# Optimization experiments

Measured on AMD Instinct MI355X. Metric: run time of the kernel, lower is better.

## Reference

```python
import jax, jax.numpy as jnp
import numpy as np

K = 3  # kernel size per dim


def _conv3d(x, w, b):
    # x: (N,C,T,H,W), w: (O,C,3,3,3), stride 1, padding 1
    y = jax.lax.conv_general_dilated(
        x, w, window_strides=(1, 1, 1),
        padding=((1, 1), (1, 1), (1, 1)),
        dimension_numbers=('NCDHW', 'OIDHW', 'NCDHW'))
    return y + b[None, :, None, None, None]


def _dcn_hw(x, w_off, b_off, w, b):
    """DeformConvPack_d with dimension='HW': offsets only along H and W."""
    N, C, T, H, W = x.shape
    KK = K * K * K  # 27 taps
    # offset prediction conv: (N, 2*27, T, H, W) -> (N, 27, 2, T, H, W)
    off = _conv3d(x, w_off, b_off).reshape(N, KK, 2, T, H, W)
    kt, kh, kw = [a.reshape(-1) for a in jnp.meshgrid(
        jnp.arange(K), jnp.arange(K), jnp.arange(K), indexing='ij')]
    # temporal sampling positions are integer (no offset along T)
    p_t = jnp.arange(T)[None, :] + kt[:, None] - 1              # (27, T)
    t_ok = ((p_t >= 0) & (p_t < T))[None, :, :, None, None]     # (1,27,T,1,1)
    p_tc = jnp.clip(p_t, 0, T - 1)[None, :, :, None, None]
    # fractional spatial sampling positions: (N,27,T,H,W)
    p_h = (jnp.arange(H, dtype=x.dtype)[None, None, None, :, None]
           + (kh - 1).astype(x.dtype)[None, :, None, None, None] + off[:, :, 0])
    p_w = (jnp.arange(W, dtype=x.dtype)[None, None, None, None, :]
           + (kw - 1).astype(x.dtype)[None, :, None, None, None] + off[:, :, 1])
    h0f = jnp.floor(p_h); w0f = jnp.floor(p_w)
    lh = (p_h - h0f)[..., None]; lw = (p_w - w0f)[..., None]
    h0 = h0f.astype(jnp.int32); w0 = w0f.astype(jnp.int32)
    xt = jnp.transpose(x, (0, 2, 3, 4, 1))  # (N,T,H,W,C) for gather
    bidx = jnp.arange(N)[:, None, None, None, None]

    def corner(hi, wi):
        ok = t_ok & (hi >= 0) & (hi < H) & (wi >= 0) & (wi < W)
        v = xt[bidx, p_tc, jnp.clip(hi, 0, H - 1), jnp.clip(wi, 0, W - 1)]
        return jnp.where(ok[..., None], v, jnp.zeros((), x.dtype))

    # bilinear interpolation with zero padding outside bounds
    samp = ((1 - lh) * (1 - lw)) * corner(h0, w0) \
         + ((1 - lh) * lw) * corner(h0, w0 + 1) \
         + (lh * (1 - lw)) * corner(h0 + 1, w0) \
         + (lh * lw) * corner(h0 + 1, w0 + 1)     # (N,27,T,H,W,C)
    O = w.shape[0]
    out = jnp.einsum('nkthwc,ock->nothw', samp, w.reshape(O, C, KK))
    return out + b[None, :, None, None, None]


def setup_inputs() -> dict:
    key = jax.random.key(0)
    ks = jax.random.split(key, 6)
    N, C, T, H, W = 1, 64, 7, 48, 48
    fan = 1.0 / np.sqrt(C * 27)
    return {
        'x': jax.random.normal(ks[0], (N, C, T, H, W), jnp.float32),
        'w_off0': jax.random.normal(ks[1], (54, C, 3, 3, 3), jnp.float32) * 0.01,
        'b_off0': jnp.zeros((54,), jnp.float32),
        'w0': jax.random.normal(ks[2], (C, C, 3, 3, 3), jnp.float32) * fan,
        'b0': jnp.zeros((C,), jnp.float32),
        'w_off1': jax.random.normal(ks[3], (54, C, 3, 3, 3), jnp.float32) * 0.01,
        'b_off1': jnp.zeros((54,), jnp.float32),
        'w1': jax.random.normal(ks[4], (C, C, 3, 3, 3), jnp.float32) * fan,
        'b1': jnp.zeros((C,), jnp.float32),
    }


def reference(x, w_off0, b_off0, w0, b0, w_off1, b_off1, w1, b1):
    h = _dcn_hw(x, w_off0, b_off0, w0, b0)
    h = jnp.where(h >= 0, h, 0.1 * h)  # LeakyReLU(0.1)
    return _dcn_hw(h, w_off1, b_off1, w1, b1) + x
```

## Files before the change

kernel.cpp:

```cpp
#include <hip/hip_runtime.h>

#define T_ 7
#define H_ 48
#define W_ 48
#define P_ 16128
#define HW_ 2304

typedef __attribute__((ext_vector_type(8))) short short8;
typedef __attribute__((ext_vector_type(4))) float f32x4;
typedef __attribute__((ext_vector_type(4))) unsigned u32x4;

__device__ __forceinline__ unsigned short f2bf(float f) {
  union { float f; unsigned u; } x{f};
  unsigned r = x.u + 0x7FFFu + ((x.u >> 16) & 1u);
  return (unsigned short)(r >> 16);
}
__device__ __forceinline__ float blo(unsigned u) {
  union { unsigned u; float f; } x{u << 16};
  return x.f;
}
__device__ __forceinline__ float bhi(unsigned u) {
  union { unsigned u; float f; } x{u & 0xFFFF0000u};
  return x.f;
}
__device__ __forceinline__ unsigned pack2(float a, float b) {
  return (unsigned)f2bf(a) | ((unsigned)f2bf(b) << 16);
}
__device__ __forceinline__ int xcd_swz(int bid, int nwg) {
  int cpx = nwg >> 3;
  return (bid & 7) * cpx + (bid >> 3);
}

__global__ void k_prep_x(const float* __restrict__ in, unsigned short* __restrict__ outb) {
  __shared__ float tile[64][65];
  int p0 = blockIdx.x * 64;
  int l = threadIdx.x & 63;
  int g = threadIdx.x >> 6;
#pragma unroll
  for (int i = 0; i < 16; ++i) {
    int c = g * 16 + i;
    tile[c][l] = in[c * P_ + p0 + l];
  }
  __syncthreads();
#pragma unroll
  for (int i = 0; i < 16; ++i) {
    int p = g * 16 + i;
    outb[(p0 + p) * 64 + l] = f2bf(tile[l][p]);
  }
}

__global__ void k_prep_w4(const float* __restrict__ s0, const float* __restrict__ s1,
                          const float* __restrict__ s2, const float* __restrict__ s3,
                          unsigned short* __restrict__ d0, unsigned short* __restrict__ d1,
                          unsigned short* __restrict__ d2, unsigned short* __restrict__ d3) {
  int y = blockIdx.y;
  const float* w = (y == 0) ? s0 : (y == 1) ? s1 : (y == 2) ? s2 : s3;
  unsigned short* wt = (y == 0) ? d0 : (y == 1) ? d1 : (y == 2) ? d2 : d3;
  int OC = (y < 2) ? 54 : 64;
  int idx = blockIdx.x * 256 + threadIdx.x;
  int j = idx & 7;
  int l = (idx >> 3) & 63;
  int kc = (idx >> 9) & 1;
  int nt = (idx >> 10) & 3;
  int k = idx >> 12;
  int o = nt * 16 + (l & 15);
  int c = kc * 32 + (l >> 4) * 8 + j;
  wt[idx] = (o < OC) ? f2bf(w[(o * 64 + c) * 27 + k]) : (unsigned short)0;
}

__global__ __launch_bounds__(256) void k_off4w(const unsigned short* __restrict__ xclb,
                                               const unsigned short* __restrict__ wAs,
                                               const float* __restrict__ boff,
                                               float* __restrict__ offt2) {
  __shared__ f32x4 red[4][4][64];
  int p0 = xcd_swz(blockIdx.x, gridDim.x) * 32;
  int t = p0 / HW_;
  int r0 = p0 - t * HW_;
  int h0r = r0 / W_;
  int w0s = r0 - h0r * W_;
  int h1r = h0r + (w0s == 32 ? 1 : 0);
  int w1s = (w0s == 32) ? 0 : w0s + 16;
  int tid = threadIdx.x;
  int lane = tid & 63, wid = tid >> 6;
  int pt = lane & 15, grp = lane >> 4;

  f32x4 zacc{0.f, 0.f, 0.f, 0.f};
  f32x4 aA0 = zacc, aA1 = zacc, aA2 = zacc, aA3 = zacc;
  f32x4 aB0 = zacc, aB1 = zacc, aB2 = zacc, aB3 = zacc;
  const short8 zero8{0, 0, 0, 0, 0, 0, 0, 0};
  int kbeg = wid * 7;

#pragma unroll
  for (int kk = 0; kk < 7; ++kk) {
    int kraw = kbeg + kk;
    int k = min(kraw, 26);
    int kt = k / 9;
    int r9 = k - kt * 9;
    int kh = r9 / 3;
    int kw = r9 - (r9 / 3) * 3;
    int t2 = t + kt - 1;
    bool tok = (kraw < 27) & ((unsigned)t2 < (unsigned)T_);
    int t2c = min(max(t2, 0), T_ - 1);

    const unsigned short* wp = wAs + (size_t)k * 4096 + lane * 8;
    short8 b00 = *(const short8*)(wp);
    short8 b01 = *(const short8*)(wp + 512);
    short8 b10 = *(const short8*)(wp + 1024);
    short8 b11 = *(const short8*)(wp + 1536);
    short8 b20 = *(const short8*)(wp + 2048);
    short8 b21 = *(const short8*)(wp + 2560);
    short8 b30 = *(const short8*)(wp + 3072);
    short8 b31 = *(const short8*)(wp + 3584);

    {
      int h2 = h0r + kh - 1;
      int w2 = w0s + pt + kw - 1;
      bool ok = tok & ((unsigned)h2 < (unsigned)H_) & ((unsigned)w2 < (unsigned)W_);
      int h2c = min(max(h2, 0), H_ - 1);
      int w2c = min(max(w2, 0), W_ - 1);
      const unsigned short* ap = xclb + ((size_t)(t2c * HW_ + h2c * W_ + w2c) * 64 + grp * 8);
      short8 a0 = *(const short8*)ap;
      short8 a1 = *(const short8*)(ap + 32);
      a0 = ok ? a0 : zero8;
      a1 = ok ? a1 : zero8;
      aA0 = __builtin_amdgcn_mfma_f32_16x16x32_bf16(a0, b00, aA0, 0, 0, 0);
      aA0 = __builtin_amdgcn_mfma_f32_16x16x32_bf16(a1, b01, aA0, 0, 0, 0);
      aA1 = __builtin_amdgcn_mfma_f32_16x16x32_bf16(a0, b10, aA1, 0, 0, 0);
      aA1 = __builtin_amdgcn_mfma_f32_16x16x32_bf16(a1, b11, aA1, 0, 0, 0);
      aA2 = __builtin_amdgcn_mfma_f32_16x16x32_bf16(a0, b20, aA2, 0, 0, 0);
      aA2 = __builtin_amdgcn_mfma_f32_16x16x32_bf16(a1, b21, aA2, 0, 0, 0);
      aA3 = __builtin_amdgcn_mfma_f32_16x16x32_bf16(a0, b30, aA3, 0, 0, 0);
      aA3 = __builtin_amdgcn_mfma_f32_16x16x32_bf16(a1, b31, aA3, 0, 0, 0);
    }
    {
      int h2 = h1r + kh - 1;
      int w2 = w1s + pt + kw - 1;
      bool ok = tok & ((unsigned)h2 < (unsigned)H_) & ((unsigned)w2 < (unsigned)W_);
      int h2c = min(max(h2, 0), H_ - 1);
      int w2c = min(max(w2, 0), W_ - 1);
      const unsigned short* ap = xclb + ((size_t)(t2c * HW_ + h2c * W_ + w2c) * 64 + grp * 8);
      short8 a0 = *(const short8*)ap;
      short8 a1 = *(const short8*)(ap + 32);
      a0 = ok ? a0 : zero8;
      a1 = ok ? a1 : zero8;
      aB0 = __builtin_amdgcn_mfma_f32_16x16x32_bf16(a0, b00, aB0, 0, 0, 0);
      aB0 = __builtin_amdgcn_mfma_f32_16x16x32_bf16(a1, b01, aB0, 0, 0, 0);
      aB1 = __builtin_amdgcn_mfma_f32_16x16x32_bf16(a0, b10, aB1, 0, 0, 0);
      aB1 = __builtin_amdgcn_mfma_f32_16x16x32_bf16(a1, b11, aB1, 0, 0, 0);
      aB2 = __builtin_amdgcn_mfma_f32_16x16x32_bf16(a0, b20, aB2, 0, 0, 0);
      aB2 = __builtin_amdgcn_mfma_f32_16x16x32_bf16(a1, b21, aB2, 0, 0, 0);
      aB3 = __builtin_amdgcn_mfma_f32_16x16x32_bf16(a0, b30, aB3, 0, 0, 0);
      aB3 = __builtin_amdgcn_mfma_f32_16x16x32_bf16(a1, b31, aB3, 0, 0, 0);
    }
  }

  int oc = wid * 16 + pt;
  float bb = (oc < 54) ? boff[oc] : 0.f;
  int kidx = oc >> 1, d = oc & 1;

  red[wid][0][lane] = aA0;
  red[wid][1][lane] = aA1;
  red[wid][2][lane] = aA2;
  red[wid][3][lane] = aA3;
  __syncthreads();
  {
    f32x4 s = red[0][wid][lane];
    s = s + red[1][wid][lane];
    s = s + red[2][wid][lane];
    s = s + red[3][wid][lane];
    if (oc < 54) {
#pragma unroll
      for (int r = 0; r < 4; ++r) {
        int p = p0 + grp * 4 + r;
        offt2[((size_t)kidx * P_ + p) * 2 + d] = s[r] + bb;
      }
    }
  }
  __syncthreads();
  red[wid][0][lane] = aB0;
  red[wid][1][lane] = aB1;
  red[wid][2][lane] = aB2;
  red[wid][3][lane] = aB3;
  __syncthreads();
  {
    f32x4 s = red[0][wid][lane];
    s = s + red[1][wid][lane];
    s = s + red[2][wid][lane];
    s = s + red[3][wid][lane];
    if (oc < 54) {
#pragma unroll
      for (int r = 0; r < 4; ++r) {
        int p = p0 + 16 + grp * 4 + r;
        offt2[((size_t)kidx * P_ + p) * 2 + d] = s[r] + bb;
      }
    }
  }
}

template <int MODE>
__global__ __launch_bounds__(256) void k_samp4w(
    const unsigned short* __restrict__ xclb, const float* __restrict__ offt2,
    const unsigned short* __restrict__ wBs, const float* __restrict__ bias,
    const float* __restrict__ resid, float* __restrict__ out32,
    unsigned short* __restrict__ outb) {
  __shared__ f32x4 red[4][4][64];
  __shared__ unsigned short sA[4][2][16][72];
  int p0 = xcd_swz(blockIdx.x, gridDim.x) * 32;
  int t = p0 / HW_;
  int r0 = p0 - t * HW_;
  int h0r = r0 / W_;
  int w0s = r0 - h0r * W_;
  int h1r = h0r + (w0s == 32 ? 1 : 0);
  int w1s = (w0s == 32) ? 0 : w0s + 16;
  int tid = threadIdx.x;
  int lane = tid & 63, wid = tid >> 6;
  int pt = lane & 15, grp = lane >> 4;

  f32x4 zacc{0.f, 0.f, 0.f, 0.f};
  f32x4 aA0 = zacc, aA1 = zacc, aA2 = zacc, aA3 = zacc;
  f32x4 aB0 = zacc, aB1 = zacc, aB2 = zacc, aB3 = zacc;
  int kbeg = wid * 7;

#pragma unroll
  for (int kk = 0; kk < 7; ++kk) {
    int kraw = kbeg + kk;
    int k = min(kraw, 26);
    int kt = k / 9;
    int r9 = k - kt * 9;
    int kh = r9 / 3;
    int kw = r9 - (r9 / 3) * 3;
    int t2 = t + kt - 1;
    bool tok = (kraw < 27) & ((unsigned)t2 < (unsigned)T_);
    int t2c = min(max(t2, 0), T_ - 1);

    const unsigned short* wp = wBs + (size_t)k * 4096 + lane * 8;
    short8 b00 = *(const short8*)(wp);
    short8 b01 = *(const short8*)(wp + 512);
    short8 b10 = *(const short8*)(wp + 1024);
    short8 b11 = *(const short8*)(wp + 1536);
    short8 b20 = *(const short8*)(wp + 2048);
    short8 b21 = *(const short8*)(wp + 2560);
    short8 b30 = *(const short8*)(wp + 3072);
    short8 b31 = *(const short8*)(wp + 3584);

#pragma unroll
    for (int f = 0; f < 2; ++f) {
      int hrow = (f == 0) ? h0r : h1r;
      int wst = (f == 0) ? w0s : w1s;
      float2 o2 = *(const float2*)(offt2 + ((size_t)k * P_ + p0 + f * 16 + pt) * 2);
      float ph = (float)(hrow + kh - 1) + o2.x;
      float pw = (float)(wst + pt + kw - 1) + o2.y;
      float hf = floorf(ph), wf = floorf(pw);
      float lh = ph - hf, lw = pw - wf;
      int h0 = (int)hf, w0i = (int)wf;
      int h1 = h0 + 1, w1 = w0i + 1;
      bool h0ok = ((unsigned)h0 < (unsigned)H_), h1ok = ((unsigned)h1 < (unsigned)H_);
      bool w0ok = ((unsigned)w0i < (unsigned)W_), w1ok = ((unsigned)w1 < (unsigned)W_);
      int h0c = min(max(h0, 0), H_ - 1), h1c = min(max(h1, 0), H_ - 1);
      int w0c = min(max(w0i, 0), W_ - 1), w1c = min(max(w1, 0), W_ - 1);
      float omlh = 1.f - lh, omlw = 1.f - lw;
      float g00 = (tok & h0ok & w0ok) ? omlh * omlw : 0.f;
      float g01 = (tok & h0ok & w1ok) ? omlh * lw : 0.f;
      float g10 = (tok & h1ok & w0ok) ? lh * omlw : 0.f;
      float g11 = (tok & h1ok & w1ok) ? lh * lw : 0.f;

      const unsigned short* bt = xclb + (size_t)(t2c * HW_) * 64 + grp * 16;
      int i00 = (h0c * W_ + w0c) * 64;
      int i01 = (h0c * W_ + w1c) * 64;
      int i10 = (h1c * W_ + w0c) * 64;
      int i11 = (h1c * W_ + w1c) * 64;
      u32x4 A0 = *(const u32x4*)(bt + i00), A1 = *(const u32x4*)(bt + i00 + 8);
      u32x4 B0 = *(const u32x4*)(bt + i01), B1 = *(const u32x4*)(bt + i01 + 8);
      u32x4 C0 = *(const u32x4*)(bt + i10), C1 = *(const u32x4*)(bt + i10 + 8);
      u32x4 D0 = *(const u32x4*)(bt + i11), D1 = *(const u32x4*)(bt + i11 + 8);

#define LERPU(a, b, c, d)                                                   \
  pack2(g00 * blo(a) + g01 * blo(b) + g10 * blo(c) + g11 * blo(d),          \
        g00 * bhi(a) + g01 * bhi(b) + g10 * bhi(c) + g11 * bhi(d))
      u32x4 v0, v1;
      v0[0] = LERPU(A0[0], B0[0], C0[0], D0[0]);
      v0[1] = LERPU(A0[1], B0[1], C0[1], D0[1]);
      v0[2] = LERPU(A0[2], B0[2], C0[2], D0[2]);
      v0[3] = LERPU(A0[3], B0[3], C0[3], D0[3]);
      v1[0] = LERPU(A1[0], B1[0], C1[0], D1[0]);
      v1[1] = LERPU(A1[1], B1[1], C1[1], D1[1]);
      v1[2] = LERPU(A1[2], B1[2], C1[2], D1[2]);
      v1[3] = LERPU(A1[3], B1[3], C1[3], D1[3]);
#undef LERPU

      __builtin_amdgcn_wave_barrier();
      *(u32x4*)&sA[wid][f][pt][grp * 16] = v0;
      *(u32x4*)&sA[wid][f][pt][grp * 16 + 8] = v1;
      __builtin_amdgcn_wave_barrier();

      short8 af0 = *(const short8*)&sA[wid][f][pt][grp * 8];
      short8 af1 = *(const short8*)&sA[wid][f][pt][32 + grp * 8];
      __builtin_amdgcn_wave_barrier();

      if (f == 0) {
        aA0 = __builtin_amdgcn_mfma_f32_16x16x32_bf16(af0, b00, aA0, 0, 0, 0);
        aA0 = __builtin_amdgcn_mfma_f32_16x16x32_bf16(af1, b01, aA0, 0, 0, 0);
        aA1 = __builtin_amdgcn_mfma_f32_16x16x32_bf16(af0, b10, aA1, 0, 0, 0);
        aA1 = __builtin_amdgcn_mfma_f32_16x16x32_bf16(af1, b11, aA1, 0, 0, 0);
        aA2 = __builtin_amdgcn_mfma_f32_16x16x32_bf16(af0, b20, aA2, 0, 0, 0);
        aA2 = __builtin_amdgcn_mfma_f32_16x16x32_bf16(af1, b21, aA2, 0, 0, 0);
        aA3 = __builtin_amdgcn_mfma_f32_16x16x32_bf16(af0, b30, aA3, 0, 0, 0);
        aA3 = __builtin_amdgcn_mfma_f32_16x16x32_bf16(af1, b31, aA3, 0, 0, 0);
      } else {
        aB0 = __builtin_amdgcn_mfma_f32_16x16x32_bf16(af0, b00, aB0, 0, 0, 0);
        aB0 = __builtin_amdgcn_mfma_f32_16x16x32_bf16(af1, b01, aB0, 0, 0, 0);
        aB1 = __builtin_amdgcn_mfma_f32_16x16x32_bf16(af0, b10, aB1, 0, 0, 0);
        aB1 = __builtin_amdgcn_mfma_f32_16x16x32_bf16(af1, b11, aB1, 0, 0, 0);
        aB2 = __builtin_amdgcn_mfma_f32_16x16x32_bf16(af0, b20, aB2, 0, 0, 0);
        aB2 = __builtin_amdgcn_mfma_f32_16x16x32_bf16(af1, b21, aB2, 0, 0, 0);
        aB3 = __builtin_amdgcn_mfma_f32_16x16x32_bf16(af0, b30, aB3, 0, 0, 0);
        aB3 = __builtin_amdgcn_mfma_f32_16x16x32_bf16(af1, b31, aB3, 0, 0, 0);
      }
    }
  }

  int ch = wid * 16 + pt;
  float bb = bias[ch];

  red[wid][0][lane] = aA0;
  red[wid][1][lane] = aA1;
  red[wid][2][lane] = aA2;
  red[wid][3][lane] = aA3;
  __syncthreads();
  {
    f32x4 s = red[0][wid][lane];
    s = s + red[1][wid][lane];
    s = s + red[2][wid][lane];
    s = s + red[3][wid][lane];
#pragma unroll
    for (int r = 0; r < 4; ++r) {
      int p = p0 + grp * 4 + r;
      float v = s[r] + bb;
      if (MODE == 0) {
        v = (v >= 0.f) ? v : 0.1f * v;
        outb[(size_t)p * 64 + ch] = f2bf(v);
      } else {
        out32[(size_t)ch * P_ + p] = v + resid[(size_t)ch * P_ + p];
      }
    }
  }
  __syncthreads();
  red[wid][0][lane] = aB0;
  red[wid][1][lane] = aB1;
  red[wid][2][lane] = aB2;
  red[wid][3][lane] = aB3;
  __syncthreads();
  {
    f32x4 s = red[0][wid][lane];
    s = s + red[1][wid][lane];
    s = s + red[2][wid][lane];
    s = s + red[3][wid][lane];
#pragma unroll
    for (int r = 0; r < 4; ++r) {
      int p = p0 + 16 + grp * 4 + r;
      float v = s[r] + bb;
      if (MODE == 0) {
        v = (v >= 0.f) ? v : 0.1f * v;
        outb[(size_t)p * 64 + ch] = f2bf(v);
      } else {
        out32[(size_t)ch * P_ + p] = v + resid[(size_t)ch * P_ + p];
      }
    }
  }
}

extern "C" void kernel_launch(void* const* d_in, const int* in_sizes, int n_in,
                              void* d_out, int out_size, void* d_ws, size_t ws_size,
                              hipStream_t stream) {
  const float* x      = (const float*)d_in[0];
  const float* w_off0 = (const float*)d_in[1];
  const float* b_off0 = (const float*)d_in[2];
  const float* w0     = (const float*)d_in[3];
  const float* b0     = (const float*)d_in[4];
  const float* w_off1 = (const float*)d_in[5];
  const float* b_off1 = (const float*)d_in[6];
  const float* w1     = (const float*)d_in[7];
  const float* b1     = (const float*)d_in[8];
  float* out = (float*)d_out;

  char* base = (char*)d_ws;
  unsigned short* x_clb = (unsigned short*)base;
  unsigned short* h_clb = (unsigned short*)(base + 2064384);
  float*          offt2 = (float*)(base + 4128768);
  unsigned short* wA0   = (unsigned short*)(base + 7612416);
  unsigned short* wA1   = (unsigned short*)(base + 7833600);
  unsigned short* wB0   = (unsigned short*)(base + 8054784);
  unsigned short* wB1   = (unsigned short*)(base + 8275968);

  hipLaunchKernelGGL(k_prep_x, dim3(252), dim3(256), 0, stream, x, x_clb);
  hipLaunchKernelGGL(k_prep_w4, dim3(432, 4), dim3(256), 0, stream,
                     w_off0, w_off1, w0, w1, wA0, wA1, wB0, wB1);

  hipLaunchKernelGGL(k_off4w, dim3(504), dim3(256), 0, stream, x_clb, wA0, b_off0, offt2);
  hipLaunchKernelGGL((k_samp4w<0>), dim3(504), dim3(256), 0, stream,
                     x_clb, offt2, wB0, b0, (const float*)nullptr, (float*)nullptr, h_clb);

  hipLaunchKernelGGL(k_off4w, dim3(504), dim3(256), 0, stream, h_clb, wA1, b_off1, offt2);
  hipLaunchKernelGGL((k_samp4w<1>), dim3(504), dim3(256), 0, stream,
                     h_clb, offt2, wB1, b1, x, out, (unsigned short*)nullptr);
}
```

Measured before the change: 99.67 us.

## Stage input row window in LDS for deformable sampling gathers

The sampling kernel now loops over the temporal tap, and for each one it cooperatively loads an 11-row by 48-column window of the bf16 input (all 64 channels) into dynamic shared memory with an XOR swizzle. The bilinear corner gathers then read from LDS, falling back to global loads only when a sampled row lies outside the window. Taps are redistributed so waves 0-2 each handle two spatial taps and wave 3 handles three. Per-tap offsets are preloaded, and the MFMA and weight loads are factored into helpers. The aim is to replace scattered global and L2 gathers with LDS reads, at the cost of about 66 KB of LDS per block, extra block barriers, lower occupancy and uneven work across waves.

```diff
diff --git a/kernel.cpp b/kernel.cpp
--- a/kernel.cpp
+++ b/kernel.cpp
@@ -5,6 +5,8 @@
 #define W_ 48
 #define P_ 16128
 #define HW_ 2304
+#define WR_ 11
+#define NCH_ (WR_ * 48 * 8)
 
 typedef __attribute__((ext_vector_type(8))) short short8;
 typedef __attribute__((ext_vector_type(4))) float f32x4;
@@ -29,6 +31,34 @@
 __device__ __forceinline__ int xcd_swz(int bid, int nwg) {
   int cpx = nwg >> 3;
   return (bid & 7) * cpx + (bid >> 3);
+}
+
+struct Wgt { short8 b00, b01, b10, b11, b20, b21, b30, b31; };
+
+__device__ __forceinline__ Wgt load_w(const unsigned short* base, int k, int lane) {
+  const unsigned short* wp = base + (size_t)k * 4096 + lane * 8;
+  Wgt w;
+  w.b00 = *(const short8*)(wp);
+  w.b01 = *(const short8*)(wp + 512);
+  w.b10 = *(const short8*)(wp + 1024);
+  w.b11 = *(const short8*)(wp + 1536);
+  w.b20 = *(const short8*)(wp + 2048);
+  w.b21 = *(const short8*)(wp + 2560);
+  w.b30 = *(const short8*)(wp + 3072);
+  w.b31 = *(const short8*)(wp + 3584);
+  return w;
+}
+
+__device__ __forceinline__ void mfma8(const Wgt& W, short8 af0, short8 af1,
+                                      f32x4& c0, f32x4& c1, f32x4& c2, f32x4& c3) {
+  c0 = __builtin_amdgcn_mfma_f32_16x16x32_bf16(af0, W.b00, c0, 0, 0, 0);
+  c0 = __builtin_amdgcn_mfma_f32_16x16x32_bf16(af1, W.b01, c0, 0, 0, 0);
+  c1 = __builtin_amdgcn_mfma_f32_16x16x32_bf16(af0, W.b10, c1, 0, 0, 0);
+  c1 = __builtin_amdgcn_mfma_f32_16x16x32_bf16(af1, W.b11, c1, 0, 0, 0);
+  c2 = __builtin_amdgcn_mfma_f32_16x16x32_bf16(af0, W.b20, c2, 0, 0, 0);
+  c2 = __builtin_amdgcn_mfma_f32_16x16x32_bf16(af1, W.b21, c2, 0, 0, 0);
+  c3 = __builtin_amdgcn_mfma_f32_16x16x32_bf16(af0, W.b30, c3, 0, 0, 0);
+  c3 = __builtin_amdgcn_mfma_f32_16x16x32_bf16(af1, W.b31, c3, 0, 0, 0);
 }
 
 __global__ void k_prep_x(const float* __restrict__ in, unsigned short* __restrict__ outb) {
@@ -102,16 +132,7 @@
     bool tok = (kraw < 27) & ((unsigned)t2 < (unsigned)T_);
     int t2c = min(max(t2, 0), T_ - 1);
 
-    const unsigned short* wp = wAs + (size_t)k * 4096 + lane * 8;
-    short8 b00 = *(const short8*)(wp);
-    short8 b01 = *(const short8*)(wp + 512);
-    short8 b10 = *(const short8*)(wp + 1024);
-    short8 b11 = *(const short8*)(wp + 1536);
-    short8 b20 = *(const short8*)(wp + 2048);
-    short8 b21 = *(const short8*)(wp + 2560);
-    short8 b30 = *(const short8*)(wp + 3072);
-    short8 b31 = *(const short8*)(wp + 3584);
-
+    Wgt W = load_w(wAs, k, lane);
     {
       int h2 = h0r + kh - 1;
       int w2 = w0s + pt + kw - 1;
@@ -123,14 +144,7 @@
       short8 a1 = *(const short8*)(ap + 32);
       a0 = ok ? a0 : zero8;
       a1 = ok ? a1 : zero8;
-      aA0 = __builtin_amdgcn_mfma_f32_16x16x32_bf16(a0, b00, aA0, 0, 0, 0);
-      aA0 = __builtin_amdgcn_mfma_f32_16x16x32_bf16(a1, b01, aA0, 0, 0, 0);
-      aA1 = __builtin_amdgcn_mfma_f32_16x16x32_bf16(a0, b10, aA1, 0, 0, 0);
-      aA1 = __builtin_amdgcn_mfma_f32_16x16x32_bf16(a1, b11, aA1, 0, 0, 0);
-      aA2 = __builtin_amdgcn_mfma_f32_16x16x32_bf16(a0, b20, aA2, 0, 0, 0);
-      aA2 = __builtin_amdgcn_mfma_f32_16x16x32_bf16(a1, b21, aA2, 0, 0, 0);
-      aA3 = __builtin_amdgcn_mfma_f32_16x16x32_bf16(a0, b30, aA3, 0, 0, 0);
-      aA3 = __builtin_amdgcn_mfma_f32_16x16x32_bf16(a1, b31, aA3, 0, 0, 0);
+      mfma8(W, a0, a1, aA0, aA1, aA2, aA3);
     }
     {
       int h2 = h1r + kh - 1;
@@ -143,14 +157,7 @@
       short8 a1 = *(const short8*)(ap + 32);
       a0 = ok ? a0 : zero8;
       a1 = ok ? a1 : zero8;
-      aB0 = __builtin_amdgcn_mfma_f32_16x16x32_bf16(a0, b00, aB0, 0, 0, 0);
-      aB0 = __builtin_amdgcn_mfma_f32_16x16x32_bf16(a1, b01, aB0, 0, 0, 0);
-      aB1 = __builtin_amdgcn_mfma_f32_16x16x32_bf16(a0, b10, aB1, 0, 0, 0);
-      aB1 = __builtin_amdgcn_mfma_f32_16x16x32_bf16(a1, b11, aB1, 0, 0, 0);
-      aB2 = __builtin_amdgcn_mfma_f32_16x16x32_bf16(a0, b20, aB2, 0, 0, 0);
-      aB2 = __builtin_amdgcn_mfma_f32_16x16x32_bf16(a1, b21, aB2, 0, 0, 0);
-      aB3 = __builtin_amdgcn_mfma_f32_16x16x32_bf16(a0, b30, aB3, 0, 0, 0);
-      aB3 = __builtin_amdgcn_mfma_f32_16x16x32_bf16(a1, b31, aB3, 0, 0, 0);
+      mfma8(W, a0, a1, aB0, aB1, aB2, aB3);
     }
   }
 
@@ -198,11 +205,12 @@
 }
 
 template <int MODE>
-__global__ __launch_bounds__(256) void k_samp4w(
+__global__ __launch_bounds__(256) void k_samp_st(
     const unsigned short* __restrict__ xclb, const float* __restrict__ offt2,
     const unsigned short* __restrict__ wBs, const float* __restrict__ bias,
     const float* __restrict__ resid, float* __restrict__ out32,
     unsigned short* __restrict__ outb) {
+  extern __shared__ u32x4 xs[];
   __shared__ f32x4 red[4][4][64];
   __shared__ unsigned short sA[4][2][16][72];
   int p0 = xcd_swz(blockIdx.x, gridDim.x) * 32;
@@ -212,6 +220,7 @@
   int w0s = r0 - h0r * W_;
   int h1r = h0r + (w0s == 32 ? 1 : 0);
   int w1s = (w0s == 32) ? 0 : w0s + 16;
+  int lo = h0r - 4;
   int tid = threadIdx.x;
   int lane = tid & 63, wid = tid >> 6;
   int pt = lane & 15, grp = lane >> 4;
@@ -219,102 +228,113 @@
   f32x4 zacc{0.f, 0.f, 0.f, 0.f};
   f32x4 aA0 = zacc, aA1 = zacc, aA2 = zacc, aA3 = zacc;
   f32x4 aB0 = zacc, aB1 = zacc, aB2 = zacc, aB3 = zacc;
-  int kbeg = wid * 7;
-
-#pragma unroll
-  for (int kk = 0; kk < 7; ++kk) {
-    int kraw = kbeg + kk;
-    int k = min(kraw, 26);
-    int kt = k / 9;
-    int r9 = k - kt * 9;
-    int kh = r9 / 3;
-    int kw = r9 - (r9 / 3) * 3;
+
+  for (int kt = 0; kt < 3; ++kt) {
     int t2 = t + kt - 1;
-    bool tok = (kraw < 27) & ((unsigned)t2 < (unsigned)T_);
+    bool tokt = (unsigned)t2 < (unsigned)T_;
     int t2c = min(max(t2, 0), T_ - 1);
 
-    const unsigned short* wp = wBs + (size_t)k * 4096 + lane * 8;
-    short8 b00 = *(const short8*)(wp);
-    short8 b01 = *(const short8*)(wp + 512);
-    short8 b10 = *(const short8*)(wp + 1024);
-    short8 b11 = *(const short8*)(wp + 1536);
-    short8 b20 = *(const short8*)(wp + 2048);
-    short8 b21 = *(const short8*)(wp + 2560);
-    short8 b30 = *(const short8*)(wp + 3072);
-    short8 b31 = *(const short8*)(wp + 3584);
-
-#pragma unroll
-    for (int f = 0; f < 2; ++f) {
-      int hrow = (f == 0) ? h0r : h1r;
-      int wst = (f == 0) ? w0s : w1s;
-      float2 o2 = *(const float2*)(offt2 + ((size_t)k * P_ + p0 + f * 16 + pt) * 2);
-      float ph = (float)(hrow + kh - 1) + o2.x;
-      float pw = (float)(wst + pt + kw - 1) + o2.y;
-      float hf = floorf(ph), wf = floorf(pw);
-      float lh = ph - hf, lw = pw - wf;
-      int h0 = (int)hf, w0i = (int)wf;
-      int h1 = h0 + 1, w1 = w0i + 1;
-      bool h0ok = ((unsigned)h0 < (unsigned)H_), h1ok = ((unsigned)h1 < (unsigned)H_);
-      bool w0ok = ((unsigned)w0i < (unsigned)W_), w1ok = ((unsigned)w1 < (unsigned)W_);
-      int h0c = min(max(h0, 0), H_ - 1), h1c = min(max(h1, 0), H_ - 1);
-      int w0c = min(max(w0i, 0), W_ - 1), w1c = min(max(w1, 0), W_ - 1);
-      float omlh = 1.f - lh, omlw = 1.f - lw;
-      float g00 = (tok & h0ok & w0ok) ? omlh * omlw : 0.f;
-      float g01 = (tok & h0ok & w1ok) ? omlh * lw : 0.f;
-      float g10 = (tok & h1ok & w0ok) ? lh * omlw : 0.f;
-      float g11 = (tok & h1ok & w1ok) ? lh * lw : 0.f;
-
-      const unsigned short* bt = xclb + (size_t)(t2c * HW_) * 64 + grp * 16;
-      int i00 = (h0c * W_ + w0c) * 64;
-      int i01 = (h0c * W_ + w1c) * 64;
-      int i10 = (h1c * W_ + w0c) * 64;
-      int i11 = (h1c * W_ + w1c) * 64;
-      u32x4 A0 = *(const u32x4*)(bt + i00), A1 = *(const u32x4*)(bt + i00 + 8);
-      u32x4 B0 = *(const u32x4*)(bt + i01), B1 = *(const u32x4*)(bt + i01 + 8);
-      u32x4 C0 = *(const u32x4*)(bt + i10), C1 = *(const u32x4*)(bt + i10 + 8);
-      u32x4 D0 = *(const u32x4*)(bt + i11), D1 = *(const u32x4*)(bt + i11 + 8);
+    float2 offp[3][2];
+#pragma unroll
+    for (int jj = 0; jj < 3; ++jj) {
+      int jcp = (wid < 3) ? (wid * 2 + min(jj, 1)) : (6 + jj);
+      size_t ob = ((size_t)(kt * 9 + jcp) * P_ + p0) * 2;
+      offp[jj][0] = *(const float2*)(offt2 + ob + (size_t)pt * 2);
+      offp[jj][1] = *(const float2*)(offt2 + ob + (size_t)(16 + pt) * 2);
+    }
+
+    __syncthreads();
+    for (int q = tid; q < NCH_; q += 256) {
+      int pidx = q >> 3;
+      int sub = q & 7;
+      int r = pidx / 48;
+      int c = pidx - r * 48;
+      int srow = min(max(lo + r, 0), H_ - 1);
+      const u32x4* src = (const u32x4*)(xclb + (size_t)(t2c * HW_ + srow * W_ + c) * 64);
+      xs[q ^ (pidx & 7)] = src[sub];
+    }
+    __syncthreads();
+
+#pragma unroll
+    for (int jj = 0; jj < 3; ++jj) {
+      bool ok_tap = (wid == 3) | (jj < 2);
+      if (ok_tap) {
+        int jc = (wid < 3) ? (wid * 2 + jj) : (6 + jj);
+        int kh = jc / 3;
+        int kw = jc - kh * 3;
+        int kk = kt * 9 + jc;
+        Wgt W = load_w(wBs, kk, lane);
+#pragma unroll
+        for (int f = 0; f < 2; ++f) {
+          int hrow = f ? h1r : h0r;
+          int wst = f ? w1s : w0s;
+          float2 o2 = offp[jj][f];
+          float ph = (float)(hrow + kh - 1) + o2.x;
+          float pw = (float)(wst + pt + kw - 1) + o2.y;
+          float hf = floorf(ph), wf = floorf(pw);
+          float lh = ph - hf, lw = pw - wf;
+          int h0 = (int)hf, w0i = (int)wf;
+          int h1 = h0 + 1, w1 = w0i + 1;
+          bool h0ok = ((unsigned)h0 < (unsigned)H_), h1ok = ((unsigned)h1 < (unsigned)H_);
+          bool w0ok = ((unsigned)w0i < (unsigned)W_), w1ok = ((unsigned)w1 < (unsigned)W_);
+          int h0c = min(max(h0, 0), H_ - 1), h1c = min(max(h1, 0), H_ - 1);
+          int w0c = min(max(w0i, 0), W_ - 1), w1c = min(max(w1, 0), W_ - 1);
+          float omlh = 1.f - lh, omlw = 1.f - lw;
+          float g00 = (tokt & h0ok & w0ok) ? omlh * omlw : 0.f;
+          float g01 = (tokt & h0ok & w1ok) ? omlh * lw : 0.f;
+          float g10 = (tokt & h1ok & w0ok) ? lh * omlw : 0.f;
+          float g11 = (tokt & h1ok & w1ok) ? lh * lw : 0.f;
+
+          int pr0 = h0c - lo, pr1 = h1c - lo;
+          bool inw = ((unsigned)pr0 < (unsigned)WR_) & ((unsigned)pr1 < (unsigned)WR_);
+          int pr0c = min(max(pr0, 0), WR_ - 1), pr1c = min(max(pr1, 0), WR_ - 1);
+          int q00 = (pr0c * 48 + w0c), q01 = (pr0c * 48 + w1c);
+          int q10 = (pr1c * 48 + w0c), q11 = (pr1c * 48 + w1c);
+          u32x4 A0 = xs[(q00 * 8 + 2 * grp) ^ (q00 & 7)];
+          u32x4 A1 = xs[(q00 * 8 + 2 * grp + 1) ^ (q00 & 7)];
+          u32x4 B0 = xs[(q01 * 8 + 2 * grp) ^ (q01 & 7)];
+          u32x4 B1 = xs[(q01 * 8 + 2 * grp + 1) ^ (q01 & 7)];
+          u32x4 C0 = xs[(q10 * 8 + 2 * grp) ^ (q10 & 7)];
+          u32x4 C1 = xs[(q10 * 8 + 2 * grp + 1) ^ (q10 & 7)];
+          u32x4 D0 = xs[(q11 * 8 + 2 * grp) ^ (q11 & 7)];
+          u32x4 D1 = xs[(q11 * 8 + 2 * grp + 1) ^ (q11 & 7)];
+          if (!__all(inw ? 1 : 0)) {
+            if (!inw) {
+              const unsigned short* bt = xclb + (size_t)(t2c * HW_) * 64 + grp * 16;
+              int i00 = (h0c * W_ + w0c) * 64, i01 = (h0c * W_ + w1c) * 64;
+              int i10 = (h1c * W_ + w0c) * 64, i11 = (h1c * W_ + w1c) * 64;
+              A0 = *(const u32x4*)(bt + i00);  A1 = *(const u32x4*)(bt + i00 + 8);
+              B0 = *(const u32x4*)(bt + i01);  B1 = *(const u32x4*)(bt + i01 + 8);
+              C0 = *(const u32x4*)(bt + i10);  C1 = *(const u32x4*)(bt + i10 + 8);
+              D0 = *(const u32x4*)(bt + i11);  D1 = *(const u32x4*)(bt + i11 + 8);
+            }
+          }
 
 #define LERPU(a, b, c, d)                                                   \
   pack2(g00 * blo(a) + g01 * blo(b) + g10 * blo(c) + g11 * blo(d),          \
         g00 * bhi(a) + g01 * bhi(b) + g10 * bhi(c) + g11 * bhi(d))
-      u32x4 v0, v1;
-      v0[0] = LERPU(A0[0], B0[0], C0[0], D0[0]);
-      v0[1] = LERPU(A0[1], B0[1], C0[1], D0[1]);
-      v0[2] = LERPU(A0[2], B0[2], C0[2], D0[2]);
-      v0[3] = LERPU(A0[3], B0[3], C0[3], D0[3]);
-      v1[0] = LERPU(A1[0], B1[0], C1[0], D1[0]);
-      v1[1] = LERPU(A1[1], B1[1], C1[1], D1[1]);
-      v1[2] = LERPU(A1[2], B1[2], C1[2], D1[2]);
-      v1[3] = LERPU(A1[3], B1[3], C1[3], D1[3]);
+          u32x4 v0, v1;
+          v0[0] = LERPU(A0[0], B0[0], C0[0], D0[0]);
+          v0[1] = LERPU(A0[1], B0[1], C0[1], D0[1]);
+          v0[2] = LERPU(A0[2], B0[2], C0[2], D0[2]);
+          v0[3] = LERPU(A0[3], B0[3], C0[3], D0[3]);
+          v1[0] = LERPU(A1[0], B1[0], C1[0], D1[0]);
+          v1[1] = LERPU(A1[1], B1[1], C1[1], D1[1]);
+          v1[2] = LERPU(A1[2], B1[2], C1[2], D1[2]);
+          v1[3] = LERPU(A1[3], B1[3], C1[3], D1[3]);
 #undef LERPU
 
-      __builtin_amdgcn_wave_barrier();
-      *(u32x4*)&sA[wid][f][pt][grp * 16] = v0;
-      *(u32x4*)&sA[wid][f][pt][grp * 16 + 8] = v1;
-      __builtin_amdgcn_wave_barrier();
-
-      short8 af0 = *(const short8*)&sA[wid][f][pt][grp * 8];
-      short8 af1 = *(const short8*)&sA[wid][f][pt][32 + grp * 8];
-      __builtin_amdgcn_wave_barrier();
-
-      if (f == 0) {
-        aA0 = __builtin_amdgcn_mfma_f32_16x16x32_bf16(af0, b00, aA0, 0, 0, 0);
-        aA0 = __builtin_amdgcn_mfma_f32_16x16x32_bf16(af1, b01, aA0, 0, 0, 0);
-        aA1 = __builtin_amdgcn_mfma_f32_16x16x32_bf16(af0, b10, aA1, 0, 0, 0);
-        aA1 = __builtin_amdgcn_mfma_f32_16x16x32_bf16(af1, b11, aA1, 0, 0, 0);
-        aA2 = __builtin_amdgcn_mfma_f32_16x16x32_bf16(af0, b20, aA2, 0, 0, 0);
-        aA2 = __builtin_amdgcn_mfma_f32_16x16x32_bf16(af1, b21, aA2, 0, 0, 0);
-        aA3 = __builtin_amdgcn_mfma_f32_16x16x32_bf16(af0, b30, aA3, 0, 0, 0);
-        aA3 = __builtin_amdgcn_mfma_f32_16x16x32_bf16(af1, b31, aA3, 0, 0, 0);
-      } else {
-        aB0 = __builtin_amdgcn_mfma_f32_16x16x32_bf16(af0, b00, aB0, 0, 0, 0);
-        aB0 = __builtin_amdgcn_mfma_f32_16x16x32_bf16(af1, b01, aB0, 0, 0, 0);
-        aB1 = __builtin_amdgcn_mfma_f32_16x16x32_bf16(af0, b10, aB1, 0, 0, 0);
-        aB1 = __builtin_amdgcn_mfma_f32_16x16x32_bf16(af1, b11, aB1, 0, 0, 0);
-        aB2 = __builtin_amdgcn_mfma_f32_16x16x32_bf16(af0, b20, aB2, 0, 0, 0);
-        aB2 = __builtin_amdgcn_mfma_f32_16x16x32_bf16(af1, b21, aB2, 0, 0, 0);
-        aB3 = __builtin_amdgcn_mfma_f32_16x16x32_bf16(af0, b30, aB3, 0, 0, 0);
-        aB3 = __builtin_amdgcn_mfma_f32_16x16x32_bf16(af1, b31, aB3, 0, 0, 0);
+          __builtin_amdgcn_wave_barrier();
+          *(u32x4*)&sA[wid][f][pt][grp * 16] = v0;
+          *(u32x4*)&sA[wid][f][pt][grp * 16 + 8] = v1;
+          __builtin_amdgcn_wave_barrier();
+          short8 af0 = *(const short8*)&sA[wid][f][pt][grp * 8];
+          short8 af1 = *(const short8*)&sA[wid][f][pt][32 + grp * 8];
+          __builtin_amdgcn_wave_barrier();
+
+          if (f == 0) mfma8(W, af0, af1, aA0, aA1, aA2, aA3);
+          else        mfma8(W, af0, af1, aB0, aB1, aB2, aB3);
+        }
       }
     }
   }
@@ -392,15 +412,17 @@
   unsigned short* wB0   = (unsigned short*)(base + 8054784);
   unsigned short* wB1   = (unsigned short*)(base + 8275968);
 
+  const int dynlds = NCH_ * 16;
+
   hipLaunchKernelGGL(k_prep_x, dim3(252), dim3(256), 0, stream, x, x_clb);
   hipLaunchKernelGGL(k_prep_w4, dim3(432, 4), dim3(256), 0, stream,
                      w_off0, w_off1, w0, w1, wA0, wA1, wB0, wB1);
 
   hipLaunchKernelGGL(k_off4w, dim3(504), dim3(256), 0, stream, x_clb, wA0, b_off0, offt2);
-  hipLaunchKernelGGL((k_samp4w<0>), dim3(504), dim3(256), 0, stream,
+  hipLaunchKernelGGL((k_samp_st<0>), dim3(504), dim3(256), dynlds, stream,
                      x_clb, offt2, wB0, b0, (const float*)nullptr, (float*)nullptr, h_clb);
 
   hipLaunchKernelGGL(k_off4w, dim3(504), dim3(256), 0, stream, h_clb, wA1, b_off1, offt2);
-  hipLaunchKernelGGL((k_samp4w<1>), dim3(504), dim3(256), 0, stream,
+  hipLaunchKernelGGL((k_samp_st<1>), dim3(504), dim3(256), dynlds, stream,
                      h_clb, offt2, wB1, b1, x, out, (unsigned short*)nullptr);
 }
```

Result: slower. 123.6 us (+24.0%).
